# Kernel tuning notes

Measured on AMD Instinct MI355X. Metric: run time of the kernel, lower is better.

## Reference

```python
import jax, jax.numpy as jnp
import numpy as np

N = 50000      # nodes
E = 800000     # edges (avg degree 16)
FV = 128       # fv_dim (input node feature dim)
H = 128        # num_hiddens
EMB = 128      # node_embed_dim
OUT = 2        # out_ch


def _glorot(k, shape):
    lim = np.sqrt(6.0 / (shape[0] + shape[1]))
    return jax.random.uniform(k, shape, jnp.float32, -lim, lim)


def setup_inputs() -> dict:
    key = jax.random.key(0)
    ks = jax.random.split(key, 8)
    x = jax.random.normal(ks[0], (N, FV), jnp.float32)
    src = jax.random.randint(ks[1], (E,), 0, N, dtype=jnp.int32)
    dst = jax.random.randint(ks[2], (E,), 0, N, dtype=jnp.int32)
    W1 = _glorot(ks[3], (FV, H)); b1 = jnp.zeros((H,), jnp.float32)
    W2 = _glorot(ks[4], (H, H));  b2 = jnp.zeros((H,), jnp.float32)
    W3 = _glorot(ks[5], (H, EMB)); b3 = jnp.zeros((EMB,), jnp.float32)
    W_out = _glorot(ks[6], (EMB, OUT)); b_out = jnp.zeros((OUT,), jnp.float32)
    return dict(x=x, src=src, dst=dst, W1=W1, b1=b1, W2=W2, b2=b2,
                W3=W3, b3=b3, W_out=W_out, b_out=b_out)


def _gcn_layer(h, src, dst, norm_src, norm_dst, W, b):
    # DGL GraphConv, norm='both': h' = D_in^{-1/2} A D_out^{-1/2} h W + b
    h = h * norm_src                                  # scale by src out-degree
    m = jax.ops.segment_sum(h[src], dst, num_segments=N)  # gather + scatter-add
    m = m * norm_dst                                  # scale by dst in-degree
    return m @ W + b


def reference(x, src, dst, W1, b1, W2, b2, W3, b3, W_out, b_out):
    ones = jnp.ones((E,), x.dtype)
    deg_out = jax.ops.segment_sum(ones, src, num_segments=N)
    deg_in = jax.ops.segment_sum(ones, dst, num_segments=N)
    norm_src = jnp.maximum(deg_out, 1.0)[:, None] ** -0.5
    norm_dst = jnp.maximum(deg_in, 1.0)[:, None] ** -0.5

    h = jax.nn.elu(_gcn_layer(x, src, dst, norm_src, norm_dst, W1, b1))
    h = jax.nn.elu(_gcn_layer(h, src, dst, norm_src, norm_dst, W2, b2))
    n_embed = _gcn_layer(h, src, dst, norm_src, norm_dst, W3, b3)  # no activation
    n_out = n_embed @ W_out + b_out
    return (n_out, n_embed)
```

## Files before the change

kernel.cpp:

```cpp
#include <hip/hip_runtime.h>

#define N_NODES 50000
#define N_EDGES 800000
#define GRID_G 782
#define NB_HIST 128
#define EPB (N_EDGES / NB_HIST)
#define WORDS 25000
#define NORMB_BLOCKS 98

typedef float f4 __attribute__((ext_vector_type(4)));

__global__ __launch_bounds__(256) void k_hist(const int* __restrict__ src,
                                              const int* __restrict__ dst,
                                              unsigned int* __restrict__ partO,
                                              unsigned int* __restrict__ partI) {
    __shared__ unsigned int h[12500];
    const int e0 = blockIdx.x * EPB;
    for (int kind = 0; kind < 2; ++kind) {
        const int* ids = kind ? dst : src;
        unsigned int* out = kind ? partI : partO;
        for (int p = 0; p < 2; ++p) {
            for (int i = threadIdx.x; i < 12500; i += 256) h[i] = 0;
            __syncthreads();
            const int base = p * 25000;
            for (int i = threadIdx.x; i < EPB; i += 256) {
                int id = ids[e0 + i] - base;
                if ((unsigned)id < 25000u)
                    atomicAdd(&h[id >> 1], (id & 1) ? 0x10000u : 1u);
            }
            __syncthreads();
            unsigned int* o = out + blockIdx.x * WORDS + p * 12500;
            for (int i = threadIdx.x; i < 12500; i += 256) o[i] = h[i];
            __syncthreads();
        }
    }
}

__global__ __launch_bounds__(256) void k_normB(const unsigned int* __restrict__ partO,
                                               const unsigned int* __restrict__ partI,
                                               float* __restrict__ norm_src,
                                               float* __restrict__ norm_dst,
                                               int* __restrict__ deg_in,
                                               int* __restrict__ partials98) {
    __shared__ int sm4[4];
    int w = blockIdx.x * 256 + threadIdx.x;
    unsigned int lo_o = 0, hi_o = 0, lo_i = 0, hi_i = 0;
    if (w < WORDS) {
        for (int b = 0; b < NB_HIST; ++b) {
            unsigned int vo = partO[b * WORDS + w];
            unsigned int vi = partI[b * WORDS + w];
            lo_o += vo & 0xFFFFu; hi_o += vo >> 16;
            lo_i += vi & 0xFFFFu; hi_i += vi >> 16;
        }
        int n0 = 2 * w;
        *(float2*)&norm_src[n0] = make_float2(rsqrtf((float)max(lo_o, 1u)),
                                              rsqrtf((float)max(hi_o, 1u)));
        *(float2*)&norm_dst[n0] = make_float2(rsqrtf((float)max(lo_i, 1u)),
                                              rsqrtf((float)max(hi_i, 1u)));
        *(int2*)&deg_in[n0] = make_int2((int)lo_i, (int)hi_i);
    }
    int v = (int)(lo_i + hi_i);
#pragma unroll
    for (int off = 32; off > 0; off >>= 1) v += __shfl_down(v, off);
    int lane = threadIdx.x & 63, wv = threadIdx.x >> 6;
    if (lane == 0) sm4[wv] = v;
    __syncthreads();
    if (threadIdx.x == 0)
        partials98[blockIdx.x] = sm4[0] + sm4[1] + sm4[2] + sm4[3];
}

__global__ __launch_bounds__(256) void k_scan(const int* __restrict__ deg_in,
                                              const int* __restrict__ partials98,
                                              int* __restrict__ row_start,
                                              int* __restrict__ cursor) {
    __shared__ int sm[256];
    __shared__ int carry_s;
    int t = threadIdx.x;
    if (t < 64) {
        int acc = 0;
        for (int i = t; i < blockIdx.x; i += 64) acc += partials98[i];
#pragma unroll
        for (int off = 32; off > 0; off >>= 1) acc += __shfl_down(acc, off);
        if (t == 0) carry_s = acc;
    }
    int n0 = blockIdx.x * 512 + t * 2;
    int a0 = 0, a1 = 0;
    if (n0 + 1 < N_NODES) {
        int2 d = *(const int2*)&deg_in[n0];
        a0 = d.x; a1 = d.y;
    } else if (n0 < N_NODES) {
        a0 = deg_in[n0];
    }
    sm[t] = a0 + a1;
    __syncthreads();
#pragma unroll
    for (int off = 1; off < 256; off <<= 1) {
        int tv = (t >= off) ? sm[t - off] : 0;
        __syncthreads();
        sm[t] += tv;
        __syncthreads();
    }
    int excl = sm[t] - (a0 + a1) + carry_s;
    if (n0 < N_NODES) { row_start[n0] = excl; cursor[n0] = excl; }
    if (n0 + 1 < N_NODES) { row_start[n0 + 1] = excl + a0; cursor[n0 + 1] = excl + a0; }
    if (blockIdx.x == 0 && t == 0) row_start[N_NODES] = N_EDGES;
}

__device__ __forceinline__ void gemm_body(const float* __restrict__ X,
                                          const float* __restrict__ W,
                                          float* __restrict__ G,
                                          float* __restrict__ Wl, int bid) {
    const int tx = threadIdx.x & 15;
    const int ty = threadIdx.x >> 4;
    const int r0 = bid * 64 + ty * 4;
    const int c0 = tx * 4;

    const float* xr[4];
#pragma unroll
    for (int i = 0; i < 4; ++i) {
        int r = r0 + i; if (r > N_NODES - 1) r = N_NODES - 1;
        xr[i] = X + (size_t)r * 128;
    }

    float acc[2][4][4] = {};
    for (int kc = 0; kc < 2; ++kc) {
        __syncthreads();
#pragma unroll
        for (int it = 0; it < 8; ++it) {
            int idx = threadIdx.x * 4 + it * 1024;
            *(float4*)&Wl[idx] = *(const float4*)&W[kc * 8192 + idx];
        }
        __syncthreads();
        const int kb = kc * 64;
#pragma unroll
        for (int kq = 0; kq < 4; ++kq) {
            float4 xa[4][4];
#pragma unroll
            for (int j = 0; j < 4; ++j)
#pragma unroll
                for (int i = 0; i < 4; ++i)
                    xa[i][j] = *(const float4*)(xr[i] + kb + kq * 16 + j * 4);
#pragma unroll
            for (int j = 0; j < 4; ++j) {
                const int ks = kq * 16 + j * 4;
#pragma unroll
                for (int kk = 0; kk < 4; ++kk) {
                    float4 w0 = *(const float4*)&Wl[(ks + kk) * 128 + c0];
                    float4 w1 = *(const float4*)&Wl[(ks + kk) * 128 + c0 + 64];
#pragma unroll
                    for (int i = 0; i < 4; ++i) {
                        float a = (kk == 0) ? xa[i][j].x : (kk == 1) ? xa[i][j].y
                                 : (kk == 2) ? xa[i][j].z : xa[i][j].w;
                        acc[0][i][0] = fmaf(a, w0.x, acc[0][i][0]);
                        acc[0][i][1] = fmaf(a, w0.y, acc[0][i][1]);
                        acc[0][i][2] = fmaf(a, w0.z, acc[0][i][2]);
                        acc[0][i][3] = fmaf(a, w0.w, acc[0][i][3]);
                        acc[1][i][0] = fmaf(a, w1.x, acc[1][i][0]);
                        acc[1][i][1] = fmaf(a, w1.y, acc[1][i][1]);
                        acc[1][i][2] = fmaf(a, w1.z, acc[1][i][2]);
                        acc[1][i][3] = fmaf(a, w1.w, acc[1][i][3]);
                    }
                }
            }
        }
    }
#pragma unroll
    for (int i = 0; i < 4; ++i) {
        int r = r0 + i;
        if (r < N_NODES) {
            f4* p = (f4*)(G + (size_t)r * 128 + c0);
            f4 v0 = {acc[0][i][0], acc[0][i][1], acc[0][i][2], acc[0][i][3]};
            f4 v1 = {acc[1][i][0], acc[1][i][1], acc[1][i][2], acc[1][i][3]};
            __builtin_nontemporal_store(v0, p);
            __builtin_nontemporal_store(v1, p + 16);
        }
    }
}

__global__ __launch_bounds__(256, 4) void k_gemm(const float* __restrict__ X,
                                                 const float* __restrict__ W,
                                                 float* __restrict__ G) {
    __shared__ float Wl[8192];
    gemm_body(X, W, G, Wl, blockIdx.x);
}

__global__ __launch_bounds__(256, 4) void k_gemm_fill(const float* __restrict__ X,
                                                      const float* __restrict__ W,
                                                      float* __restrict__ G,
                                                      const int* __restrict__ src,
                                                      const int* __restrict__ dst,
                                                      const float* __restrict__ norm_src,
                                                      int* __restrict__ cursor,
                                                      int2* __restrict__ csr) {
    __shared__ float Wl[8192];
    if (blockIdx.x < GRID_G) {
        gemm_body(X, W, G, Wl, blockIdx.x);
    } else {
        int e = (blockIdx.x - GRID_G) * 256 + threadIdx.x;
        if (e < N_EDGES) {
            int d = dst[e], s = src[e];
            int pos = atomicAdd(&cursor[d], 1);
            csr[pos] = make_int2(s, __float_as_int(norm_src[s]));
        }
    }
}

template <int ELU, int PROJ>
__global__ __launch_bounds__(256) void k_gather(const float* __restrict__ G,
                                                const int* __restrict__ row_start,
                                                const int2* __restrict__ csr,
                                                const float* __restrict__ norm_dst,
                                                const float* __restrict__ bias,
                                                float* __restrict__ Out,
                                                const float* __restrict__ Wo,
                                                const float* __restrict__ bo,
                                                float* __restrict__ proj_out) {
    int n = (blockIdx.x * 256 + threadIdx.x) >> 6;
    int lane = threadIdx.x & 63;
    if (n >= N_NODES) return;
    const int half = lane >> 5;
    const int l = lane & 31;
    int e0 = row_start[n], e1 = row_start[n + 1];
    float4 a0 = {0,0,0,0}, a1 = {0,0,0,0}, a2 = {0,0,0,0}, a3 = {0,0,0,0};
    int e = e0;
    for (; e + 8 <= e1; e += 8) {
        int2 c0 = csr[e + half],     c1 = csr[e + 2 + half];
        int2 c2 = csr[e + 4 + half], c3 = csr[e + 6 + half];
        float4 g0 = *(const float4*)(G + (size_t)c0.x * 128 + l * 4);
        float4 g1 = *(const float4*)(G + (size_t)c1.x * 128 + l * 4);
        float4 g2 = *(const float4*)(G + (size_t)c2.x * 128 + l * 4);
        float4 g3 = *(const float4*)(G + (size_t)c3.x * 128 + l * 4);
        float w0 = __int_as_float(c0.y), w1 = __int_as_float(c1.y);
        float w2 = __int_as_float(c2.y), w3 = __int_as_float(c3.y);
        a0.x = fmaf(w0, g0.x, a0.x); a0.y = fmaf(w0, g0.y, a0.y);
        a0.z = fmaf(w0, g0.z, a0.z); a0.w = fmaf(w0, g0.w, a0.w);
        a1.x = fmaf(w1, g1.x, a1.x); a1.y = fmaf(w1, g1.y, a1.y);
        a1.z = fmaf(w1, g1.z, a1.z); a1.w = fmaf(w1, g1.w, a1.w);
        a2.x = fmaf(w2, g2.x, a2.x); a2.y = fmaf(w2, g2.y, a2.y);
        a2.z = fmaf(w2, g2.z, a2.z); a2.w = fmaf(w2, g2.w, a2.w);
        a3.x = fmaf(w3, g3.x, a3.x); a3.y = fmaf(w3, g3.y, a3.y);
        a3.z = fmaf(w3, g3.z, a3.z); a3.w = fmaf(w3, g3.w, a3.w);
    }
    for (; e < e1; e += 2) {
        int idx = e + half;
        if (idx < e1) {
            int2 c = csr[idx];
            float w = __int_as_float(c.y);
            float4 g = *(const float4*)(G + (size_t)c.x * 128 + l * 4);
            a0.x = fmaf(w, g.x, a0.x); a0.y = fmaf(w, g.y, a0.y);
            a0.z = fmaf(w, g.z, a0.z); a0.w = fmaf(w, g.w, a0.w);
        }
    }
    float4 s;
    s.x = (a0.x + a1.x) + (a2.x + a3.x);
    s.y = (a0.y + a1.y) + (a2.y + a3.y);
    s.z = (a0.z + a1.z) + (a2.z + a3.z);
    s.w = (a0.w + a1.w) + (a2.w + a3.w);
    s.x += __shfl_xor(s.x, 32);
    s.y += __shfl_xor(s.y, 32);
    s.z += __shfl_xor(s.z, 32);
    s.w += __shfl_xor(s.w, 32);
    float nd = norm_dst[n];
    float4 b = *(const float4*)(bias + l * 4);
    float4 o;
    o.x = fmaf(nd, s.x, b.x);
    o.y = fmaf(nd, s.y, b.y);
    o.z = fmaf(nd, s.z, b.z);
    o.w = fmaf(nd, s.w, b.w);
    if (ELU) {
        o.x = o.x > 0.f ? o.x : expm1f(o.x);
        o.y = o.y > 0.f ? o.y : expm1f(o.y);
        o.z = o.z > 0.f ? o.z : expm1f(o.z);
        o.w = o.w > 0.f ? o.w : expm1f(o.w);
    }
    if (half == 0)
        *(float4*)(Out + (size_t)n * 128 + l * 4) = o;
    if (PROJ) {
        float p0 = o.x * Wo[(l * 4 + 0) * 2] + o.y * Wo[(l * 4 + 1) * 2]
                 + o.z * Wo[(l * 4 + 2) * 2] + o.w * Wo[(l * 4 + 3) * 2];
        float p1 = o.x * Wo[(l * 4 + 0) * 2 + 1] + o.y * Wo[(l * 4 + 1) * 2 + 1]
                 + o.z * Wo[(l * 4 + 2) * 2 + 1] + o.w * Wo[(l * 4 + 3) * 2 + 1];
#pragma unroll
        for (int off = 16; off > 0; off >>= 1) {
            p0 += __shfl_down(p0, off);
            p1 += __shfl_down(p1, off);
        }
        if (lane == 0) {
            proj_out[n * 2 + 0] = p0 + bo[0];
            proj_out[n * 2 + 1] = p1 + bo[1];
        }
    }
}

extern "C" void kernel_launch(void* const* d_in, const int* in_sizes, int n_in,
                              void* d_out, int out_size, void* d_ws, size_t ws_size,
                              hipStream_t stream) {
    const float* x     = (const float*)d_in[0];
    const int*   src   = (const int*)d_in[1];
    const int*   dst   = (const int*)d_in[2];
    const float* W1    = (const float*)d_in[3];
    const float* b1    = (const float*)d_in[4];
    const float* W2    = (const float*)d_in[5];
    const float* b2    = (const float*)d_in[6];
    const float* W3    = (const float*)d_in[7];
    const float* b3    = (const float*)d_in[8];
    const float* W_out = (const float*)d_in[9];
    const float* b_out = (const float*)d_in[10];

    float* out = (float*)d_out;
    float* emb = out + (size_t)N_NODES * 2;

    char* ws = (char*)d_ws;
    float* norm_src  = (float*)(ws + 0);
    float* norm_dst  = (float*)(ws + 200192);
    int*   deg_in    = (int*)(ws + 400384);
    int*   row_start = (int*)(ws + 600576);
    int*   cursor    = (int*)(ws + 801280);
    int*   partials98= (int*)(ws + 1001472);
    int2*  csr       = (int2*)(ws + 1001984);
    float* bufA      = (float*)(ws + 7401984);
    float* bufB      = (float*)(ws + 33001984);
    unsigned int* partO = (unsigned int*)bufA;
    unsigned int* partI = partO + (size_t)NB_HIST * WORDS;

    const int gridW = (N_NODES * 64 + 255) / 256;
    const int gridF = GRID_G + (N_EDGES + 255) / 256;

    k_hist<<<NB_HIST, 256, 0, stream>>>(src, dst, partO, partI);
    k_normB<<<NORMB_BLOCKS, 256, 0, stream>>>(partO, partI, norm_src, norm_dst,
                                              deg_in, partials98);
    k_scan<<<NORMB_BLOCKS, 256, 0, stream>>>(deg_in, partials98, row_start, cursor);
    k_gemm_fill<<<gridF, 256, 0, stream>>>(x, W1, bufB, src, dst, norm_src,
                                           cursor, csr);
    k_gather<1, 0><<<gridW, 256, 0, stream>>>(bufB, row_start, csr, norm_dst, b1,
                                              bufA, nullptr, nullptr, nullptr);
    k_gemm<<<GRID_G, 256, 0, stream>>>(bufA, W2, bufB);
    k_gather<1, 0><<<gridW, 256, 0, stream>>>(bufB, row_start, csr, norm_dst, b2,
                                              bufA, nullptr, nullptr, nullptr);
    k_gemm<<<GRID_G, 256, 0, stream>>>(bufA, W3, bufB);
    k_gather<0, 1><<<gridW, 256, 0, stream>>>(bufB, row_start, csr, norm_dst, b3,
                                              emb, W_out, b_out, out);
}
```

Measured before the change: 323.4 us.

## Double-buffer X and W tiles in LDS via async global_load_lds in GEMM

```diff
diff --git a/kernel.cpp b/kernel.cpp
--- a/kernel.cpp
+++ b/kernel.cpp
@@ -106,63 +106,78 @@
     if (blockIdx.x == 0 && t == 0) row_start[N_NODES] = N_EDGES;
 }
 
+__device__ __forceinline__ void stage_chunk(const float* __restrict__ X,
+                                            const float* __restrict__ W,
+                                            float* Xl, float* Wl,
+                                            int bid, int kc, int tid) {
+    const int wv = tid >> 6, l = tid & 63;
+#pragma unroll
+    for (int j = 0; j < 2; ++j) {
+        int rl = wv * 16 + j * 8 + (l >> 3);
+        int r = bid * 64 + rl; if (r > N_NODES - 1) r = N_NODES - 1;
+        const float* g = X + (size_t)r * 128 + kc * 32 + (l & 7) * 4;
+        float* d = Xl + (wv * 16 + j * 8) * 32;
+        __builtin_amdgcn_global_load_lds((__attribute__((address_space(1))) void*)g,
+                                         (__attribute__((address_space(3))) void*)d,
+                                         16, 0, 0);
+    }
+#pragma unroll
+    for (int j = 0; j < 4; ++j) {
+        const float* g = W + kc * 4096 + (wv * 4 + j) * 256 + l * 4;
+        float* d = Wl + (wv * 4 + j) * 256;
+        __builtin_amdgcn_global_load_lds((__attribute__((address_space(1))) void*)g,
+                                         (__attribute__((address_space(3))) void*)d,
+                                         16, 0, 0);
+    }
+}
+
 __device__ __forceinline__ void gemm_body(const float* __restrict__ X,
                                           const float* __restrict__ W,
                                           float* __restrict__ G,
-                                          float* __restrict__ Wl, int bid) {
-    const int tx = threadIdx.x & 15;
-    const int ty = threadIdx.x >> 4;
+                                          float* Xl0, float* Xl1,
+                                          float* Wl0, float* Wl1, int bid) {
+    const int tid = threadIdx.x;
+    const int tx = tid & 15;
+    const int ty = tid >> 4;
     const int r0 = bid * 64 + ty * 4;
     const int c0 = tx * 4;
 
-    const float* xr[4];
-#pragma unroll
-    for (int i = 0; i < 4; ++i) {
-        int r = r0 + i; if (r > N_NODES - 1) r = N_NODES - 1;
-        xr[i] = X + (size_t)r * 128;
-    }
-
     float acc[2][4][4] = {};
-    for (int kc = 0; kc < 2; ++kc) {
-        __syncthreads();
-#pragma unroll
-        for (int it = 0; it < 8; ++it) {
-            int idx = threadIdx.x * 4 + it * 1024;
-            *(float4*)&Wl[idx] = *(const float4*)&W[kc * 8192 + idx];
-        }
-        __syncthreads();
-        const int kb = kc * 64;
-#pragma unroll
-        for (int kq = 0; kq < 4; ++kq) {
-            float4 xa[4][4];
-#pragma unroll
-            for (int j = 0; j < 4; ++j)
-#pragma unroll
-                for (int i = 0; i < 4; ++i)
-                    xa[i][j] = *(const float4*)(xr[i] + kb + kq * 16 + j * 4);
-#pragma unroll
-            for (int j = 0; j < 4; ++j) {
-                const int ks = kq * 16 + j * 4;
-#pragma unroll
-                for (int kk = 0; kk < 4; ++kk) {
-                    float4 w0 = *(const float4*)&Wl[(ks + kk) * 128 + c0];
-                    float4 w1 = *(const float4*)&Wl[(ks + kk) * 128 + c0 + 64];
-#pragma unroll
-                    for (int i = 0; i < 4; ++i) {
-                        float a = (kk == 0) ? xa[i][j].x : (kk == 1) ? xa[i][j].y
-                                 : (kk == 2) ? xa[i][j].z : xa[i][j].w;
-                        acc[0][i][0] = fmaf(a, w0.x, acc[0][i][0]);
-                        acc[0][i][1] = fmaf(a, w0.y, acc[0][i][1]);
-                        acc[0][i][2] = fmaf(a, w0.z, acc[0][i][2]);
-                        acc[0][i][3] = fmaf(a, w0.w, acc[0][i][3]);
-                        acc[1][i][0] = fmaf(a, w1.x, acc[1][i][0]);
-                        acc[1][i][1] = fmaf(a, w1.y, acc[1][i][1]);
-                        acc[1][i][2] = fmaf(a, w1.z, acc[1][i][2]);
-                        acc[1][i][3] = fmaf(a, w1.w, acc[1][i][3]);
-                    }
+    stage_chunk(X, W, Xl0, Wl0, bid, 0, tid);
+    __syncthreads();
+
+#pragma unroll
+    for (int kc = 0; kc < 4; ++kc) {
+        float* Xcur = (kc & 1) ? Xl1 : Xl0;
+        float* Wcur = (kc & 1) ? Wl1 : Wl0;
+        if (kc < 3)
+            stage_chunk(X, W, (kc & 1) ? Xl0 : Xl1, (kc & 1) ? Wl0 : Wl1, bid, kc + 1, tid);
+#pragma unroll 2
+        for (int ks = 0; ks < 32; ks += 4) {
+            float4 xa[4];
+#pragma unroll
+            for (int i = 0; i < 4; ++i)
+                xa[i] = *(const float4*)&Xcur[(ty * 4 + i) * 32 + ks];
+#pragma unroll
+            for (int kk = 0; kk < 4; ++kk) {
+                float4 w0 = *(const float4*)&Wcur[(ks + kk) * 128 + c0];
+                float4 w1 = *(const float4*)&Wcur[(ks + kk) * 128 + c0 + 64];
+#pragma unroll
+                for (int i = 0; i < 4; ++i) {
+                    float a = (kk == 0) ? xa[i].x : (kk == 1) ? xa[i].y
+                             : (kk == 2) ? xa[i].z : xa[i].w;
+                    acc[0][i][0] = fmaf(a, w0.x, acc[0][i][0]);
+                    acc[0][i][1] = fmaf(a, w0.y, acc[0][i][1]);
+                    acc[0][i][2] = fmaf(a, w0.z, acc[0][i][2]);
+                    acc[0][i][3] = fmaf(a, w0.w, acc[0][i][3]);
+                    acc[1][i][0] = fmaf(a, w1.x, acc[1][i][0]);
+                    acc[1][i][1] = fmaf(a, w1.y, acc[1][i][1]);
+                    acc[1][i][2] = fmaf(a, w1.z, acc[1][i][2]);
+                    acc[1][i][3] = fmaf(a, w1.w, acc[1][i][3]);
                 }
             }
         }
+        __syncthreads();
     }
 #pragma unroll
     for (int i = 0; i < 4; ++i) {
@@ -180,8 +195,9 @@
 __global__ __launch_bounds__(256, 4) void k_gemm(const float* __restrict__ X,
                                                  const float* __restrict__ W,
                                                  float* __restrict__ G) {
-    __shared__ float Wl[8192];
-    gemm_body(X, W, G, Wl, blockIdx.x);
+    __shared__ float Xl[2][2048];
+    __shared__ float Wl[2][4096];
+    gemm_body(X, W, G, &Xl[0][0], &Xl[1][0], &Wl[0][0], &Wl[1][0], blockIdx.x);
 }
 
 __global__ __launch_bounds__(256, 4) void k_gemm_fill(const float* __restrict__ X,
@@ -192,9 +208,10 @@
                                                       const float* __restrict__ norm_src,
                                                       int* __restrict__ cursor,
                                                       int2* __restrict__ csr) {
-    __shared__ float Wl[8192];
+    __shared__ float Xl[2][2048];
+    __shared__ float Wl[2][4096];
     if (blockIdx.x < GRID_G) {
-        gemm_body(X, W, G, Wl, blockIdx.x);
+        gemm_body(X, W, G, &Xl[0][0], &Xl[1][0], &Wl[0][0], &Wl[1][0], blockIdx.x);
     } else {
         int e = (blockIdx.x - GRID_G) * 256 + threadIdx.x;
         if (e < N_EDGES) {
```

After: 343.1 us. +6.1%, slower.
